# Kernel optimization log

Hardware: AMD Instinct MI355X
Metric: run time of the kernel (lower is better)

## Reference

```python
import jax, jax.numpy as jnp
import numpy as np

T, H, I, E, K = 4096, 2048, 1408, 8, 2


def setup_inputs() -> dict:
    key = jax.random.key(0)
    k1, k2, k3, k4, k5, k6 = jax.random.split(key, 6)
    hidden_states = jax.random.normal(k1, (T, H), dtype=jnp.float32)
    top_k_index = jax.random.randint(k2, (T, K), 0, E, dtype=jnp.int32)
    top_k_weights = jax.random.uniform(k3, (T, K), dtype=jnp.float32)
    # nn.Linear stores weight as [out_features, in_features]
    s_h = 1.0 / np.sqrt(H)
    s_i = 1.0 / np.sqrt(I)
    gate_w = jax.random.uniform(k4, (E, I, H), dtype=jnp.float32, minval=-s_h, maxval=s_h)
    up_w = jax.random.uniform(k5, (E, I, H), dtype=jnp.float32, minval=-s_h, maxval=s_h)
    down_w = jax.random.uniform(k6, (E, H, I), dtype=jnp.float32, minval=-s_i, maxval=s_i)
    return {
        "hidden_states": hidden_states,
        "top_k_index": top_k_index,
        "top_k_weights": top_k_weights,
        "gate_w": gate_w,
        "up_w": up_w,
        "down_w": down_w,
    }


def reference(hidden_states, top_k_index, top_k_weights, gate_w, up_w, down_w):
    # combine[t, e] = sum_k top_k_weights[t, k] * 1[top_k_index[t, k] == e]
    num_experts = gate_w.shape[0]
    one_hot = jax.nn.one_hot(top_k_index, num_experts, dtype=hidden_states.dtype)  # [T, K, E]
    combine = jnp.einsum("tk,tke->te", top_k_weights, one_hot)  # [T, E]

    # dense-equivalent of per-expert gather -> SwiGLU MLP -> scatter-add
    gate = jnp.einsum("th,eih->tei", hidden_states, gate_w)  # [T, E, I]
    up = jnp.einsum("th,eih->tei", hidden_states, up_w)      # [T, E, I]
    inter = jax.nn.silu(gate) * up                               # [T, E, I]
    out = jnp.einsum("te,tei,ehi->th", combine, inter, down_w)  # [T, H]
    return out
```

## Files before the change

### kernel.cpp

```cpp
#include <hip/hip_runtime.h>
#include <cstdint>
#include <cstddef>

#define T_TOK 4096
#define HD 2048
#define ID 1408
#define NE 8
#define NA (T_TOK * 2)
#define MAXR 10240
#define MAXT 40
#define EIH ((size_t)NE * ID * HD)
#define N4 ((int)(EIH / 4))
#define NCGU 2048
#define NCASTD 512
#define NTILE_G (MAXR / 256)
#define NGEMM_GU (NTILE_G * (ID / 128))
#define NKGU (HD / 32)
#define NKD  (ID / 32)

typedef __bf16 bf16x8 __attribute__((ext_vector_type(8)));
typedef float f32x4 __attribute__((ext_vector_type(4)));

__device__ __forceinline__ unsigned short f2bf(float f) {
  union { float f; unsigned int u; } c; c.f = f;
  unsigned int u = c.u;
  u += 0x7fffu + ((u >> 16) & 1u);
  return (unsigned short)(u >> 16);
}

__device__ __forceinline__ void gl_lds16(const unsigned short* g, unsigned short* l) {
  __builtin_amdgcn_global_load_lds(
      (const __attribute__((address_space(1))) unsigned int*)g,
      (__attribute__((address_space(3))) unsigned int*)l, 16, 0, 0);
}

__device__ __forceinline__ int swz_off(int R, int fq) {
  int q = ((R & 1) << 2) | fq;
  int p = q ^ ((R >> 1) & 7);
  return (R >> 1) * 64 + p * 8;
}

__global__ void moe_count(const int* __restrict__ idx, int* __restrict__ cnt) {
  int a = blockIdx.x * 256 + threadIdx.x;
  if (a < NA) atomicAdd(&cnt[idx[a]], 1);
}

__global__ void moe_scan(const int* __restrict__ cnt, int* __restrict__ seg,
                         int* __restrict__ work_e, int* __restrict__ work_r,
                         int* __restrict__ ntiles) {
  if (blockIdx.x == 0 && threadIdx.x == 0) {
    int off = 0, nt = 0;
    for (int e = 0; e < NE; ++e) {
      seg[e] = off;
      int c = cnt[e];
      int tiles = (c + 255) >> 8;
      for (int tb = 0; tb < tiles; ++tb) {
        work_e[nt] = e;
        work_r[nt] = off + tb * 256;
        ++nt;
      }
      off += tiles << 8;
    }
    *ntiles = nt;
  }
}

__global__ void moe_fill(const int* __restrict__ idx, const float* __restrict__ wts,
                         const int* __restrict__ seg, int* __restrict__ cnt2,
                         int* __restrict__ row_token, float* __restrict__ row_weight,
                         int* __restrict__ slot_of) {
  int a = blockIdx.x * 256 + threadIdx.x;
  if (a < NA) {
    int e = idx[a];
    int pos = atomicAdd(&cnt2[e], 1);
    int slot = seg[e] + pos;
    row_token[slot] = a >> 1;
    row_weight[slot] = wts[a];
    slot_of[a] = slot;
  }
}

__global__ void mega_gather_castgu(
    const float* __restrict__ hidden, const int* __restrict__ slot_of,
    unsigned short* __restrict__ Xg,
    const float* __restrict__ gate_w, const float* __restrict__ up_w,
    unsigned short* __restrict__ gate_bf, unsigned short* __restrict__ ub_out) {
  const int bx = blockIdx.x;
  if (bx < NA) {
    const int slot = slot_of[bx];
    const int t = bx >> 1;
    const float4* src = (const float4*)(hidden + (size_t)t * HD);
    ushort4* dst = (ushort4*)(Xg + (size_t)slot * HD);
#pragma unroll
    for (int j = 0; j < 2; ++j) {
      int i = threadIdx.x + j * 256;
      float4 v = src[i];
      ushort4 o;
      o.x = f2bf(v.x); o.y = f2bf(v.y); o.z = f2bf(v.z); o.w = f2bf(v.w);
      dst[i] = o;
    }
  } else {
    const int cb = bx - NA;
    const int total = 2 * N4;
    for (int i = cb * 256 + threadIdx.x; i < total; i += NCGU * 256) {
      const float* s; unsigned short* t; int j = i;
      if (j < N4) { s = gate_w; t = gate_bf; }
      else { s = up_w; t = ub_out; j -= N4; }
      f32x4 v = __builtin_nontemporal_load((const f32x4*)s + j);
      ushort4 o;
      o.x = f2bf(v[0]); o.y = f2bf(v[1]); o.z = f2bf(v[2]); o.w = f2bf(v[3]);
      ((ushort4*)t)[j] = o;
    }
  }
}

__global__ __launch_bounds__(512, 2) void moe_gateup(
    const unsigned short* __restrict__ Xg,
    const unsigned short* __restrict__ Wg,
    const unsigned short* __restrict__ Wu,
    unsigned short* __restrict__ inter,
    const int* __restrict__ work_e, const int* __restrict__ work_r,
    const int* __restrict__ ntiles,
    const float* __restrict__ down_w, unsigned short* __restrict__ down_bf) {
  const int bx = blockIdx.x;
  if (bx >= NGEMM_GU) {
    const int cb = bx - NGEMM_GU;
    for (int i = cb * 512 + threadIdx.x; i < N4; i += NCASTD * 512) {
      f32x4 v = __builtin_nontemporal_load((const f32x4*)down_w + i);
      ushort4 o;
      o.x = f2bf(v[0]); o.y = f2bf(v[1]); o.z = f2bf(v[2]); o.w = f2bf(v[3]);
      ((ushort4*)down_bf)[i] = o;
    }
    return;
  }
  const int g = (bx & 7) * (NGEMM_GU / 8) + (bx >> 3);
  const int tile = g % NTILE_G;
  if (tile >= *ntiles) return;
  const int e = work_e[tile];
  const int row0 = work_r[tile];
  const int col0 = (g / NTILE_G) * 128;

  __shared__ unsigned short As[3][256 * 32];
  __shared__ unsigned short Bs[3][256 * 32];

  const int tid = threadIdx.x;
  const int lane = tid & 63;
  const int wave = tid >> 6;
  const int wm = wave >> 2, wn = wave & 3;
  const int p_l = lane & 7;
  const int ub  = lane >> 3;
  const int q_l = p_l ^ ub;
  const int srow = (ub << 1) | (q_l >> 2);
  const int scol = (q_l & 3) << 3;
  const int fm = lane & 15, fq = lane >> 4;

  const size_t a_base = (size_t)row0 * HD;
  const size_t b_base = ((size_t)e * ID + col0) * HD;

  f32x4 zero = {0.f, 0.f, 0.f, 0.f};
  f32x4 accg[8][2], accu[8][2];
#pragma unroll
  for (int mi = 0; mi < 8; ++mi)
#pragma unroll
    for (int ni = 0; ni < 2; ++ni) { accg[mi][ni] = zero; accu[mi][ni] = zero; }

  auto stageA = [&](int k0, int b) {
#pragma unroll
    for (int j = 0; j < 2; ++j) {
      const int rb = j * 128 + wave * 16;
      gl_lds16(Xg + a_base + (size_t)(rb + srow) * HD + k0 + scol, &As[b][rb * 32]);
    }
  };
  auto stageB = [&](int k0, int b) {
    const int rb = wave * 16;
    gl_lds16(Wg + b_base + (size_t)(rb + srow) * HD + k0 + scol, &Bs[b][rb * 32]);
    gl_lds16(Wu + b_base + (size_t)(rb + srow) * HD + k0 + scol, &Bs[b][(128 + rb) * 32]);
  };

  stageA(0, 0); stageB(0, 0);
  stageA(32, 1); stageB(32, 1);
  asm volatile("s_waitcnt vmcnt(4)" ::: "memory");
  __builtin_amdgcn_s_barrier();
  __builtin_amdgcn_sched_barrier(0);

  int bufc = 0, buf2 = 2, k2 = 64;
  bf16x8 bg[2], bu[2];
#pragma unroll 1
  for (int t = 0; t < NKGU; ++t) {
    if (t + 2 < NKGU) stageA(k2, buf2);
    {
      bf16x8 af[4];
#pragma unroll
      for (int i = 0; i < 2; ++i) {
        bg[i] = *(const bf16x8*)&Bs[bufc][swz_off(wn * 32 + i * 16 + fm, fq)];
        bu[i] = *(const bf16x8*)&Bs[bufc][swz_off(128 + wn * 32 + i * 16 + fm, fq)];
      }
#pragma unroll
      for (int i = 0; i < 4; ++i)
        af[i] = *(const bf16x8*)&As[bufc][swz_off(wm * 128 + i * 16 + fm, fq)];
      __builtin_amdgcn_s_setprio(1);
#pragma unroll
      for (int mi = 0; mi < 4; ++mi)
#pragma unroll
        for (int ni = 0; ni < 2; ++ni) {
          accg[mi][ni] = __builtin_amdgcn_mfma_f32_16x16x32_bf16(af[mi], bg[ni], accg[mi][ni], 0, 0, 0);
          accu[mi][ni] = __builtin_amdgcn_mfma_f32_16x16x32_bf16(af[mi], bu[ni], accu[mi][ni], 0, 0, 0);
        }
      __builtin_amdgcn_s_setprio(0);
    }
    __builtin_amdgcn_s_barrier();
    __builtin_amdgcn_sched_barrier(0);
    if (t + 2 < NKGU) stageB(k2, buf2);
    {
      bf16x8 af[4];
#pragma unroll
      for (int i = 0; i < 4; ++i)
        af[i] = *(const bf16x8*)&As[bufc][swz_off(wm * 128 + (4 + i) * 16 + fm, fq)];
      __builtin_amdgcn_s_setprio(1);
#pragma unroll
      for (int mi = 0; mi < 4; ++mi)
#pragma unroll
        for (int ni = 0; ni < 2; ++ni) {
          accg[4 + mi][ni] = __builtin_amdgcn_mfma_f32_16x16x32_bf16(af[mi], bg[ni], accg[4 + mi][ni], 0, 0, 0);
          accu[4 + mi][ni] = __builtin_amdgcn_mfma_f32_16x16x32_bf16(af[mi], bu[ni], accu[4 + mi][ni], 0, 0, 0);
        }
      __builtin_amdgcn_s_setprio(0);
    }
    if (t < NKGU - 1) {
      if (t + 2 < NKGU) asm volatile("s_waitcnt vmcnt(4)" ::: "memory");
      else              asm volatile("s_waitcnt vmcnt(0)" ::: "memory");
      __builtin_amdgcn_s_barrier();
      __builtin_amdgcn_sched_barrier(0);
    }
    k2 += 32;
    bufc = (bufc == 2) ? 0 : bufc + 1;
    buf2 = (buf2 == 2) ? 0 : buf2 + 1;
  }

#pragma unroll
  for (int mi = 0; mi < 8; ++mi)
#pragma unroll
    for (int ni = 0; ni < 2; ++ni)
#pragma unroll
      for (int r = 0; r < 4; ++r) {
        float gg = accg[mi][ni][r];
        float u = accu[mi][ni][r];
        float v = (gg / (1.0f + __expf(-gg))) * u;
        int row = row0 + wm * 128 + mi * 16 + fq * 4 + r;
        int col = col0 + wn * 32 + ni * 16 + fm;
        inter[(size_t)row * ID + col] = f2bf(v);
      }
}

__global__ __launch_bounds__(512, 2) void moe_down(
    const unsigned short* __restrict__ inter,
    const unsigned short* __restrict__ Wd,
    float* __restrict__ out,
    const int* __restrict__ work_e, const int* __restrict__ work_r,
    const int* __restrict__ ntiles,
    const int* __restrict__ row_token, const float* __restrict__ row_weight) {
  const int tile = blockIdx.x;
  if (tile >= *ntiles) return;
  const int e = work_e[tile];
  const int row0 = work_r[tile];
  const int col0 = blockIdx.y * 256;

  __shared__ unsigned short As[3][256 * 32];
  __shared__ unsigned short Bs[3][256 * 32];
  __shared__ int tok_s[256];
  __shared__ float w_s[256];

  const int tid = threadIdx.x;
  if (tid < 256) {
    tok_s[tid] = row_token[row0 + tid];
    w_s[tid] = row_weight[row0 + tid];
  }
  __syncthreads();

  const int lane = tid & 63;
  const int wave = tid >> 6;
  const int wm = wave >> 2, wn = wave & 3;
  const int p_l = lane & 7;
  const int ub  = lane >> 3;
  const int q_l = p_l ^ ub;
  const int srow = (ub << 1) | (q_l >> 2);
  const int scol = (q_l & 3) << 3;
  const int fm = lane & 15, fq = lane >> 4;

  const size_t a_base = (size_t)row0 * ID;
  const size_t b_base = ((size_t)e * HD + col0) * ID;

  f32x4 zero = {0.f, 0.f, 0.f, 0.f};
  f32x4 acc[8][4];
#pragma unroll
  for (int mi = 0; mi < 8; ++mi)
#pragma unroll
    for (int ni = 0; ni < 4; ++ni) acc[mi][ni] = zero;

  auto stageA = [&](int k0, int b) {
#pragma unroll
    for (int j = 0; j < 2; ++j) {
      const int rb = j * 128 + wave * 16;
      gl_lds16(inter + a_base + (size_t)(rb + srow) * ID + k0 + scol, &As[b][rb * 32]);
    }
  };
  auto stageB = [&](int k0, int b) {
#pragma unroll
    for (int j = 0; j < 2; ++j) {
      const int rb = j * 128 + wave * 16;
      gl_lds16(Wd + b_base + (size_t)(rb + srow) * ID + k0 + scol, &Bs[b][rb * 32]);
    }
  };

  stageA(0, 0); stageB(0, 0);
  stageA(32, 1); stageB(32, 1);
  asm volatile("s_waitcnt vmcnt(4)" ::: "memory");
  __builtin_amdgcn_s_barrier();
  __builtin_amdgcn_sched_barrier(0);

  int bufc = 0, buf2 = 2, k2 = 64;
  bf16x8 b4[4];
#pragma unroll 1
  for (int t = 0; t < NKD; ++t) {
    if (t + 2 < NKD) stageA(k2, buf2);
    {
      bf16x8 af[4];
#pragma unroll
      for (int i = 0; i < 4; ++i)
        b4[i] = *(const bf16x8*)&Bs[bufc][swz_off(wn * 64 + i * 16 + fm, fq)];
#pragma unroll
      for (int i = 0; i < 4; ++i)
        af[i] = *(const bf16x8*)&As[bufc][swz_off(wm * 128 + i * 16 + fm, fq)];
      __builtin_amdgcn_s_setprio(1);
#pragma unroll
      for (int mi = 0; mi < 4; ++mi)
#pragma unroll
        for (int ni = 0; ni < 4; ++ni)
          acc[mi][ni] = __builtin_amdgcn_mfma_f32_16x16x32_bf16(af[mi], b4[ni], acc[mi][ni], 0, 0, 0);
      __builtin_amdgcn_s_setprio(0);
    }
    __builtin_amdgcn_s_barrier();
    __builtin_amdgcn_sched_barrier(0);
    if (t + 2 < NKD) stageB(k2, buf2);
    {
      bf16x8 af[4];
#pragma unroll
      for (int i = 0; i < 4; ++i)
        af[i] = *(const bf16x8*)&As[bufc][swz_off(wm * 128 + (4 + i) * 16 + fm, fq)];
      __builtin_amdgcn_s_setprio(1);
#pragma unroll
      for (int mi = 0; mi < 4; ++mi)
#pragma unroll
        for (int ni = 0; ni < 4; ++ni)
          acc[4 + mi][ni] = __builtin_amdgcn_mfma_f32_16x16x32_bf16(af[mi], b4[ni], acc[4 + mi][ni], 0, 0, 0);
      __builtin_amdgcn_s_setprio(0);
    }
    if (t < NKD - 1) {
      if (t + 2 < NKD) asm volatile("s_waitcnt vmcnt(4)" ::: "memory");
      else             asm volatile("s_waitcnt vmcnt(0)" ::: "memory");
      __builtin_amdgcn_s_barrier();
      __builtin_amdgcn_sched_barrier(0);
    }
    k2 += 32;
    bufc = (bufc == 2) ? 0 : bufc + 1;
    buf2 = (buf2 == 2) ? 0 : buf2 + 1;
  }

#pragma unroll
  for (int mi = 0; mi < 8; ++mi)
#pragma unroll
    for (int ni = 0; ni < 4; ++ni)
#pragma unroll
      for (int r = 0; r < 4; ++r) {
        int rl = wm * 128 + mi * 16 + fq * 4 + r;
        int tok = tok_s[rl];
        if (tok >= 0) {
          int col = col0 + wn * 64 + ni * 16 + fm;
          atomicAdd(&out[(size_t)tok * HD + col], w_s[rl] * acc[mi][ni][r]);
        }
      }
}

extern "C" void kernel_launch(void* const* d_in, const int* in_sizes, int n_in,
                              void* d_out, int out_size, void* d_ws, size_t ws_size,
                              hipStream_t stream) {
  const float* hidden = (const float*)d_in[0];
  const int* topk_idx = (const int*)d_in[1];
  const float* topk_w = (const float*)d_in[2];
  const float* gate_w = (const float*)d_in[3];
  const float* up_w = (const float*)d_in[4];
  const float* down_w = (const float*)d_in[5];
  float* out = (float*)d_out;

  char* ws = (char*)d_ws;
  size_t o_gate = 0;
  size_t o_up   = o_gate + EIH * 2;
  size_t o_down = o_up + EIH * 2;
  size_t o_xg   = o_down + EIH * 2;
  size_t o_int  = o_xg + (size_t)MAXR * HD * 2;
  size_t o_tok  = o_int + (size_t)MAXR * ID * 2;
  size_t o_wgt  = o_tok + (size_t)MAXR * 4;
  size_t o_slot = o_wgt + (size_t)MAXR * 4;
  size_t o_small = o_slot + (size_t)NA * 4;

  unsigned short* gate_bf = (unsigned short*)(ws + o_gate);
  unsigned short* up_bf   = (unsigned short*)(ws + o_up);
  unsigned short* down_bf = (unsigned short*)(ws + o_down);
  unsigned short* Xg      = (unsigned short*)(ws + o_xg);
  unsigned short* inter   = (unsigned short*)(ws + o_int);
  int* row_token = (int*)(ws + o_tok);
  float* row_weight = (float*)(ws + o_wgt);
  int* slot_of = (int*)(ws + o_slot);
  int* cnt    = (int*)(ws + o_small);
  int* cnt2   = cnt + 8;
  int* seg    = cnt + 16;
  int* ntiles = cnt + 24;
  int* work_e = cnt + 32;
  int* work_r = cnt + 32 + MAXT;

  hipMemsetAsync(out, 0, (size_t)T_TOK * HD * 4, stream);
  hipMemsetAsync(cnt, 0, (32 + 2 * MAXT) * 4, stream);
  hipMemsetAsync(row_token, 0xFF, (size_t)MAXR * 4, stream);

  moe_count<<<NA / 256, 256, 0, stream>>>(topk_idx, cnt);
  moe_scan<<<1, 64, 0, stream>>>(cnt, seg, work_e, work_r, ntiles);
  moe_fill<<<NA / 256, 256, 0, stream>>>(topk_idx, topk_w, seg, cnt2,
                                         row_token, row_weight, slot_of);

  mega_gather_castgu<<<NA + NCGU, 256, 0, stream>>>(hidden, slot_of, Xg,
                                                    gate_w, up_w, gate_bf, up_bf);

  moe_gateup<<<NGEMM_GU + NCASTD, 512, 0, stream>>>(
      Xg, gate_bf, up_bf, inter, work_e, work_r, ntiles, down_w, down_bf);

  dim3 gridB(NTILE_G, HD / 256);
  moe_down<<<gridB, 512, 0, stream>>>(inter, down_bf, out, work_e, work_r, ntiles,
                                      row_token, row_weight);
}
```

Measured before the change: 652.1 us.

## Double waves per GEMM block, halving per-wave rows and merging staging

Both grouped GEMM kernels now launch 1024-thread blocks with the same 256-row tile. Each of the 16 waves owns 64 rows instead of 128, which halves the accumulator count and lets A and B be staged together with one barrier per k-step instead of two. The down-cast tail block count is halved to match the larger blocks. The aim is more latency hiding and fewer barriers per step. The cost is that launch_bounds(1024,4) asks for an occupancy that forces a very small per-thread register budget, which risks spills, and LDS use limits how many blocks can actually be resident.

```diff
diff --git a/kernel.cpp b/kernel.cpp
--- a/kernel.cpp
+++ b/kernel.cpp
@@ -12,7 +12,7 @@
 #define EIH ((size_t)NE * ID * HD)
 #define N4 ((int)(EIH / 4))
 #define NCGU 2048
-#define NCASTD 512
+#define NCASTD 256
 #define NTILE_G (MAXR / 256)
 #define NGEMM_GU (NTILE_G * (ID / 128))
 #define NKGU (HD / 32)
@@ -114,7 +114,7 @@
   }
 }
 
-__global__ __launch_bounds__(512, 2) void moe_gateup(
+__global__ __launch_bounds__(1024, 4) void moe_gateup(
     const unsigned short* __restrict__ Xg,
     const unsigned short* __restrict__ Wg,
     const unsigned short* __restrict__ Wu,
@@ -125,7 +125,7 @@
   const int bx = blockIdx.x;
   if (bx >= NGEMM_GU) {
     const int cb = bx - NGEMM_GU;
-    for (int i = cb * 512 + threadIdx.x; i < N4; i += NCASTD * 512) {
+    for (int i = cb * 1024 + threadIdx.x; i < N4; i += NCASTD * 1024) {
       f32x4 v = __builtin_nontemporal_load((const f32x4*)down_w + i);
       ushort4 o;
       o.x = f2bf(v[0]); o.y = f2bf(v[1]); o.z = f2bf(v[2]); o.w = f2bf(v[3]);
@@ -156,40 +156,37 @@
 
   const size_t a_base = (size_t)row0 * HD;
   const size_t b_base = ((size_t)e * ID + col0) * HD;
+  const int rb = wave << 4;
 
   f32x4 zero = {0.f, 0.f, 0.f, 0.f};
-  f32x4 accg[8][2], accu[8][2];
-#pragma unroll
-  for (int mi = 0; mi < 8; ++mi)
+  f32x4 accg[4][2], accu[4][2];
+#pragma unroll
+  for (int mi = 0; mi < 4; ++mi)
 #pragma unroll
     for (int ni = 0; ni < 2; ++ni) { accg[mi][ni] = zero; accu[mi][ni] = zero; }
 
   auto stageA = [&](int k0, int b) {
-#pragma unroll
-    for (int j = 0; j < 2; ++j) {
-      const int rb = j * 128 + wave * 16;
-      gl_lds16(Xg + a_base + (size_t)(rb + srow) * HD + k0 + scol, &As[b][rb * 32]);
-    }
+    gl_lds16(Xg + a_base + (size_t)(rb + srow) * HD + k0 + scol, &As[b][rb * 32]);
   };
   auto stageB = [&](int k0, int b) {
-    const int rb = wave * 16;
-    gl_lds16(Wg + b_base + (size_t)(rb + srow) * HD + k0 + scol, &Bs[b][rb * 32]);
-    gl_lds16(Wu + b_base + (size_t)(rb + srow) * HD + k0 + scol, &Bs[b][(128 + rb) * 32]);
+    const unsigned short* src = (wave < 8)
+        ? (Wg + b_base + (size_t)(rb + srow) * HD + k0 + scol)
+        : (Wu + b_base + (size_t)(rb - 128 + srow) * HD + k0 + scol);
+    gl_lds16(src, &Bs[b][rb * 32]);
   };
 
   stageA(0, 0); stageB(0, 0);
   stageA(32, 1); stageB(32, 1);
-  asm volatile("s_waitcnt vmcnt(4)" ::: "memory");
+  asm volatile("s_waitcnt vmcnt(2)" ::: "memory");
   __builtin_amdgcn_s_barrier();
   __builtin_amdgcn_sched_barrier(0);
 
   int bufc = 0, buf2 = 2, k2 = 64;
-  bf16x8 bg[2], bu[2];
 #pragma unroll 1
   for (int t = 0; t < NKGU; ++t) {
-    if (t + 2 < NKGU) stageA(k2, buf2);
+    if (t + 2 < NKGU) { stageA(k2, buf2); stageB(k2, buf2); }
     {
-      bf16x8 af[4];
+      bf16x8 af[4], bg[2], bu[2];
 #pragma unroll
       for (int i = 0; i < 2; ++i) {
         bg[i] = *(const bf16x8*)&Bs[bufc][swz_off(wn * 32 + i * 16 + fm, fq)];
@@ -197,7 +194,7 @@
       }
 #pragma unroll
       for (int i = 0; i < 4; ++i)
-        af[i] = *(const bf16x8*)&As[bufc][swz_off(wm * 128 + i * 16 + fm, fq)];
+        af[i] = *(const bf16x8*)&As[bufc][swz_off(wm * 64 + i * 16 + fm, fq)];
       __builtin_amdgcn_s_setprio(1);
 #pragma unroll
       for (int mi = 0; mi < 4; ++mi)
@@ -208,26 +205,8 @@
         }
       __builtin_amdgcn_s_setprio(0);
     }
-    __builtin_amdgcn_s_barrier();
-    __builtin_amdgcn_sched_barrier(0);
-    if (t + 2 < NKGU) stageB(k2, buf2);
-    {
-      bf16x8 af[4];
-#pragma unroll
-      for (int i = 0; i < 4; ++i)
-        af[i] = *(const bf16x8*)&As[bufc][swz_off(wm * 128 + (4 + i) * 16 + fm, fq)];
-      __builtin_amdgcn_s_setprio(1);
-#pragma unroll
-      for (int mi = 0; mi < 4; ++mi)
-#pragma unroll
-        for (int ni = 0; ni < 2; ++ni) {
-          accg[4 + mi][ni] = __builtin_amdgcn_mfma_f32_16x16x32_bf16(af[mi], bg[ni], accg[4 + mi][ni], 0, 0, 0);
-          accu[4 + mi][ni] = __builtin_amdgcn_mfma_f32_16x16x32_bf16(af[mi], bu[ni], accu[4 + mi][ni], 0, 0, 0);
-        }
-      __builtin_amdgcn_s_setprio(0);
-    }
     if (t < NKGU - 1) {
-      if (t + 2 < NKGU) asm volatile("s_waitcnt vmcnt(4)" ::: "memory");
+      if (t + 2 < NKGU) asm volatile("s_waitcnt vmcnt(2)" ::: "memory");
       else              asm volatile("s_waitcnt vmcnt(0)" ::: "memory");
       __builtin_amdgcn_s_barrier();
       __builtin_amdgcn_sched_barrier(0);
@@ -238,7 +217,7 @@
   }
 
 #pragma unroll
-  for (int mi = 0; mi < 8; ++mi)
+  for (int mi = 0; mi < 4; ++mi)
 #pragma unroll
     for (int ni = 0; ni < 2; ++ni)
 #pragma unroll
@@ -246,13 +225,13 @@
         float gg = accg[mi][ni][r];
         float u = accu[mi][ni][r];
         float v = (gg / (1.0f + __expf(-gg))) * u;
-        int row = row0 + wm * 128 + mi * 16 + fq * 4 + r;
+        int row = row0 + wm * 64 + mi * 16 + fq * 4 + r;
         int col = col0 + wn * 32 + ni * 16 + fm;
         inter[(size_t)row * ID + col] = f2bf(v);
       }
 }
 
-__global__ __launch_bounds__(512, 2) void moe_down(
+__global__ __launch_bounds__(1024, 4) void moe_down(
     const unsigned short* __restrict__ inter,
     const unsigned short* __restrict__ Wd,
     float* __restrict__ out,
@@ -275,7 +254,6 @@
     tok_s[tid] = row_token[row0 + tid];
     w_s[tid] = row_weight[row0 + tid];
   }
-  __syncthreads();
 
   const int lane = tid & 63;
   const int wave = tid >> 6;
@@ -289,48 +267,40 @@
 
   const size_t a_base = (size_t)row0 * ID;
   const size_t b_base = ((size_t)e * HD + col0) * ID;
+  const int rb = wave << 4;
 
   f32x4 zero = {0.f, 0.f, 0.f, 0.f};
-  f32x4 acc[8][4];
-#pragma unroll
-  for (int mi = 0; mi < 8; ++mi)
+  f32x4 acc[4][4];
+#pragma unroll
+  for (int mi = 0; mi < 4; ++mi)
 #pragma unroll
     for (int ni = 0; ni < 4; ++ni) acc[mi][ni] = zero;
 
   auto stageA = [&](int k0, int b) {
-#pragma unroll
-    for (int j = 0; j < 2; ++j) {
-      const int rb = j * 128 + wave * 16;
-      gl_lds16(inter + a_base + (size_t)(rb + srow) * ID + k0 + scol, &As[b][rb * 32]);
-    }
+    gl_lds16(inter + a_base + (size_t)(rb + srow) * ID + k0 + scol, &As[b][rb * 32]);
   };
   auto stageB = [&](int k0, int b) {
-#pragma unroll
-    for (int j = 0; j < 2; ++j) {
-      const int rb = j * 128 + wave * 16;
-      gl_lds16(Wd + b_base + (size_t)(rb + srow) * ID + k0 + scol, &Bs[b][rb * 32]);
-    }
+    gl_lds16(Wd + b_base + (size_t)(rb + srow) * ID + k0 + scol, &Bs[b][rb * 32]);
   };
 
   stageA(0, 0); stageB(0, 0);
   stageA(32, 1); stageB(32, 1);
-  asm volatile("s_waitcnt vmcnt(4)" ::: "memory");
+  asm volatile("s_waitcnt vmcnt(2)" ::: "memory");
   __builtin_amdgcn_s_barrier();
   __builtin_amdgcn_sched_barrier(0);
 
   int bufc = 0, buf2 = 2, k2 = 64;
-  bf16x8 b4[4];
 #pragma unroll 1
   for (int t = 0; t < NKD; ++t) {
-    if (t + 2 < NKD) stageA(k2, buf2);
+    if (t + 2 < NKD) { stageA(k2, buf2); stageB(k2, buf2); }
     {
-      bf16x8 af[4];
+      bf16x8 af[4], b4[4];
 #pragma unroll
       for (int i = 0; i < 4; ++i)
         b4[i] = *(const bf16x8*)&Bs[bufc][swz_off(wn * 64 + i * 16 + fm, fq)];
 #pragma unroll
       for (int i = 0; i < 4; ++i)
-        af[i] = *(const bf16x8*)&As[bufc][swz_off(wm * 128 + i * 16 + fm, fq)];
+        af[i] = *(const bf16x8*)&As[bufc][swz_off(wm * 64 + i * 16 + fm, fq)];
       __builtin_amdgcn_s_setprio(1);
 #pragma unroll
       for (int mi = 0; mi < 4; ++mi)
@@ -339,24 +309,8 @@
           acc[mi][ni] = __builtin_amdgcn_mfma_f32_16x16x32_bf16(af[mi], b4[ni], acc[mi][ni], 0, 0, 0);
       __builtin_amdgcn_s_setprio(0);
     }
-    __builtin_amdgcn_s_barrier();
-    __builtin_amdgcn_sched_barrier(0);
-    if (t + 2 < NKD) stageB(k2, buf2);
-    {
-      bf16x8 af[4];
-#pragma unroll
-      for (int i = 0; i < 4; ++i)
-        af[i] = *(const bf16x8*)&As[bufc][swz_off(wm * 128 + (4 + i) * 16 + fm, fq)];
-      __builtin_amdgcn_s_setprio(1);
-#pragma unroll
-      for (int mi = 0; mi < 4; ++mi)
-#pragma unroll
-        for (int ni = 0; ni < 4; ++ni)
-          acc[4 + mi][ni] = __builtin_amdgcn_mfma_f32_16x16x32_bf16(af[mi], b4[ni], acc[4 + mi][ni], 0, 0, 0);
-      __builtin_amdgcn_s_setprio(0);
-    }
     if (t < NKD - 1) {
-      if (t + 2 < NKD) asm volatile("s_waitcnt vmcnt(4)" ::: "memory");
+      if (t + 2 < NKD) asm volatile("s_waitcnt vmcnt(2)" ::: "memory");
       else             asm volatile("s_waitcnt vmcnt(0)" ::: "memory");
       __builtin_amdgcn_s_barrier();
       __builtin_amdgcn_sched_barrier(0);
@@ -367,12 +321,12 @@
   }
 
 #pragma unroll
-  for (int mi = 0; mi < 8; ++mi)
+  for (int mi = 0; mi < 4; ++mi)
 #pragma unroll
     for (int ni = 0; ni < 4; ++ni)
 #pragma unroll
       for (int r = 0; r < 4; ++r) {
-        int rl = wm * 128 + mi * 16 + fq * 4 + r;
+        int rl = wm * 64 + mi * 16 + fq * 4 + r;
         int tok = tok_s[rl];
         if (tok >= 0) {
           int col = col0 + wn * 64 + ni * 16 + fm;
@@ -430,10 +384,10 @@
   mega_gather_castgu<<<NA + NCGU, 256, 0, stream>>>(hidden, slot_of, Xg,
                                                     gate_w, up_w, gate_bf, up_bf);
 
-  moe_gateup<<<NGEMM_GU + NCASTD, 512, 0, stream>>>(
+  moe_gateup<<<NGEMM_GU + NCASTD, 1024, 0, stream>>>(
       Xg, gate_bf, up_bf, inter, work_e, work_r, ntiles, down_w, down_bf);
 
   dim3 gridB(NTILE_G, HD / 256);
-  moe_down<<<gridB, 512, 0, stream>>>(inter, down_bf, out, work_e, work_r, ntiles,
-                                      row_token, row_weight);
-}
+  moe_down<<<gridB, 1024, 0, stream>>>(inter, down_bf, out, work_e, work_r, ntiles,
+                                       row_token, row_weight);
+}
```

Measured after the change: 629.5 us. 3.5% less time.

## Restructure MoE GEMM mainloops to BK=64 double-buffered four-phase ping-pong schedule

Applied to the files above, without the earlier changes.

Both the gate/up and down GEMM kernels move from a triple-buffered K=32 pipeline to a double-buffered K=64 pipeline. Each iteration is split into four phases, and each phase issues one quarter of the next tile's global-to-LDS loads and then runs one quadrant of MFMAs, with barriers and waitcnts in between. The goal is to halve loop overhead and barrier count per unit of K and to interleave loads with compute more finely. In exchange there are more barriers per iteration and a riskier ordering. The __syncthreads after the tok_s/w_s load in the down kernel is dropped and now relies on later barriers.

```diff
diff --git a/kernel.cpp b/kernel.cpp
--- a/kernel.cpp
+++ b/kernel.cpp
@@ -15,11 +15,14 @@
 #define NCASTD 512
 #define NTILE_G (MAXR / 256)
 #define NGEMM_GU (NTILE_G * (ID / 128))
-#define NKGU (HD / 32)
-#define NKD  (ID / 32)
+#define NKGU (HD / 64)
+#define NKD  (ID / 64)
 
 typedef __bf16 bf16x8 __attribute__((ext_vector_type(8)));
 typedef float f32x4 __attribute__((ext_vector_type(4)));
+
+#define MFMA16 __builtin_amdgcn_mfma_f32_16x16x32_bf16
+#define LD8(base, off) (*(const bf16x8*)&(base)[(off)])
 
 __device__ __forceinline__ unsigned short f2bf(float f) {
   union { float f; unsigned int u; } c; c.f = f;
@@ -38,6 +41,9 @@
   int q = ((R & 1) << 2) | fq;
   int p = q ^ ((R >> 1) & 7);
   return (R >> 1) * 64 + p * 8;
+}
+__device__ __forceinline__ int lds_off(int ks, int P, int fq) {
+  return ks * 8192 + swz_off(P, fq);
 }
 
 __global__ void moe_count(const int* __restrict__ idx, int* __restrict__ cnt) {
@@ -140,8 +146,8 @@
   const int row0 = work_r[tile];
   const int col0 = (g / NTILE_G) * 128;
 
-  __shared__ unsigned short As[3][256 * 32];
-  __shared__ unsigned short Bs[3][256 * 32];
+  __shared__ unsigned short As[2][16384];
+  __shared__ unsigned short Bs[2][16384];
 
   const int tid = threadIdx.x;
   const int lane = tid & 63;
@@ -162,92 +168,133 @@
 #pragma unroll
   for (int mi = 0; mi < 8; ++mi)
 #pragma unroll
-    for (int ni = 0; ni < 2; ++ni) { accg[mi][ni] = zero; accu[mi][ni] = zero; }
-
-  auto stageA = [&](int k0, int b) {
-#pragma unroll
-    for (int j = 0; j < 2; ++j) {
-      const int rb = j * 128 + wave * 16;
-      gl_lds16(Xg + a_base + (size_t)(rb + srow) * HD + k0 + scol, &As[b][rb * 32]);
-    }
+    for (int j = 0; j < 2; ++j) { accg[mi][j] = zero; accu[mi][j] = zero; }
+
+  auto stA = [&](int k0, int b, int h) {
+    const int abase = ((wave >> 2) << 7) + (h << 6) + ((wave & 3) << 4);
+    const int pp = (h << 7) + (wave << 4);
+#pragma unroll
+    for (int s = 0; s < 2; ++s)
+      gl_lds16(Xg + a_base + (size_t)(abase + srow) * HD + k0 + s * 32 + scol,
+               &As[b][s * 8192 + pp * 32]);
   };
-  auto stageB = [&](int k0, int b) {
-    const int rb = wave * 16;
-    gl_lds16(Wg + b_base + (size_t)(rb + srow) * HD + k0 + scol, &Bs[b][rb * 32]);
-    gl_lds16(Wu + b_base + (size_t)(rb + srow) * HD + k0 + scol, &Bs[b][(128 + rb) * 32]);
+  auto stB = [&](int k0, int b, int h) {
+    const unsigned short* W = h ? Wu : Wg;
+    const int pp = (h << 7) + (wave << 4);
+#pragma unroll
+    for (int s = 0; s < 2; ++s)
+      gl_lds16(W + b_base + (size_t)((wave << 4) + srow) * HD + k0 + s * 32 + scol,
+               &Bs[b][s * 8192 + pp * 32]);
   };
 
-  stageA(0, 0); stageB(0, 0);
-  stageA(32, 1); stageB(32, 1);
+  stA(0, 0, 0); stB(0, 0, 0); stB(0, 0, 1); stA(0, 0, 1);
   asm volatile("s_waitcnt vmcnt(4)" ::: "memory");
   __builtin_amdgcn_s_barrier();
-  __builtin_amdgcn_sched_barrier(0);
-
-  int bufc = 0, buf2 = 2, k2 = 64;
-  bf16x8 bg[2], bu[2];
+
+  bf16x8 a[4][2], bg[2][2], bu[2][2];
 #pragma unroll 1
   for (int t = 0; t < NKGU; ++t) {
-    if (t + 2 < NKGU) stageA(k2, buf2);
-    {
-      bf16x8 af[4];
-#pragma unroll
-      for (int i = 0; i < 2; ++i) {
-        bg[i] = *(const bf16x8*)&Bs[bufc][swz_off(wn * 32 + i * 16 + fm, fq)];
-        bu[i] = *(const bf16x8*)&Bs[bufc][swz_off(128 + wn * 32 + i * 16 + fm, fq)];
-      }
-#pragma unroll
-      for (int i = 0; i < 4; ++i)
-        af[i] = *(const bf16x8*)&As[bufc][swz_off(wm * 128 + i * 16 + fm, fq)];
-      __builtin_amdgcn_s_setprio(1);
-#pragma unroll
-      for (int mi = 0; mi < 4; ++mi)
-#pragma unroll
-        for (int ni = 0; ni < 2; ++ni) {
-          accg[mi][ni] = __builtin_amdgcn_mfma_f32_16x16x32_bf16(af[mi], bg[ni], accg[mi][ni], 0, 0, 0);
-          accu[mi][ni] = __builtin_amdgcn_mfma_f32_16x16x32_bf16(af[mi], bu[ni], accu[mi][ni], 0, 0, 0);
-        }
-      __builtin_amdgcn_s_setprio(0);
-    }
-    __builtin_amdgcn_s_barrier();
+    const int k1 = (t + 1) << 6;
+    const bool pf = (t + 1 < NKGU);
+    const unsigned short* Ab = As[t & 1];
+    const unsigned short* Bb = Bs[t & 1];
+    const int bn = (t & 1) ^ 1;
+
+#pragma unroll
+    for (int i = 0; i < 4; ++i)
+#pragma unroll
+      for (int ks = 0; ks < 2; ++ks)
+        a[i][ks] = LD8(Ab, lds_off(ks, wm * 64 + i * 16 + fm, fq));
+#pragma unroll
+    for (int j = 0; j < 2; ++j)
+#pragma unroll
+      for (int ks = 0; ks < 2; ++ks)
+        bg[j][ks] = LD8(Bb, lds_off(ks, wn * 32 + j * 16 + fm, fq));
+    if (pf) stA(k1, bn, 0);
+    __builtin_amdgcn_s_barrier();
+    asm volatile("s_waitcnt lgkmcnt(0)" ::: "memory");
     __builtin_amdgcn_sched_barrier(0);
-    if (t + 2 < NKGU) stageB(k2, buf2);
-    {
-      bf16x8 af[4];
-#pragma unroll
-      for (int i = 0; i < 4; ++i)
-        af[i] = *(const bf16x8*)&As[bufc][swz_off(wm * 128 + (4 + i) * 16 + fm, fq)];
-      __builtin_amdgcn_s_setprio(1);
-#pragma unroll
-      for (int mi = 0; mi < 4; ++mi)
-#pragma unroll
-        for (int ni = 0; ni < 2; ++ni) {
-          accg[4 + mi][ni] = __builtin_amdgcn_mfma_f32_16x16x32_bf16(af[mi], bg[ni], accg[4 + mi][ni], 0, 0, 0);
-          accu[4 + mi][ni] = __builtin_amdgcn_mfma_f32_16x16x32_bf16(af[mi], bu[ni], accu[4 + mi][ni], 0, 0, 0);
-        }
-      __builtin_amdgcn_s_setprio(0);
-    }
-    if (t < NKGU - 1) {
-      if (t + 2 < NKGU) asm volatile("s_waitcnt vmcnt(4)" ::: "memory");
-      else              asm volatile("s_waitcnt vmcnt(0)" ::: "memory");
-      __builtin_amdgcn_s_barrier();
-      __builtin_amdgcn_sched_barrier(0);
-    }
-    k2 += 32;
-    bufc = (bufc == 2) ? 0 : bufc + 1;
-    buf2 = (buf2 == 2) ? 0 : buf2 + 1;
+    __builtin_amdgcn_s_setprio(1);
+#pragma unroll
+    for (int mi = 0; mi < 4; ++mi)
+#pragma unroll
+      for (int j = 0; j < 2; ++j)
+#pragma unroll
+        for (int ks = 0; ks < 2; ++ks)
+          accg[mi][j] = MFMA16(a[mi][ks], bg[j][ks], accg[mi][j], 0, 0, 0);
+    __builtin_amdgcn_s_setprio(0);
+    if (pf) asm volatile("s_waitcnt vmcnt(4)" ::: "memory");
+    else    asm volatile("s_waitcnt vmcnt(2)" ::: "memory");
+    __builtin_amdgcn_s_barrier();
+
+#pragma unroll
+    for (int j = 0; j < 2; ++j)
+#pragma unroll
+      for (int ks = 0; ks < 2; ++ks)
+        bu[j][ks] = LD8(Bb, lds_off(ks, 128 + wn * 32 + j * 16 + fm, fq));
+    if (pf) stB(k1, bn, 0);
+    __builtin_amdgcn_s_barrier();
+    asm volatile("s_waitcnt lgkmcnt(0)" ::: "memory");
+    __builtin_amdgcn_sched_barrier(0);
+    __builtin_amdgcn_s_setprio(1);
+#pragma unroll
+    for (int mi = 0; mi < 4; ++mi)
+#pragma unroll
+      for (int j = 0; j < 2; ++j)
+#pragma unroll
+        for (int ks = 0; ks < 2; ++ks)
+          accu[mi][j] = MFMA16(a[mi][ks], bu[j][ks], accu[mi][j], 0, 0, 0);
+    __builtin_amdgcn_s_setprio(0);
+    if (pf) asm volatile("s_waitcnt vmcnt(4)" ::: "memory");
+    else    asm volatile("s_waitcnt vmcnt(0)" ::: "memory");
+    __builtin_amdgcn_s_barrier();
+
+#pragma unroll
+    for (int i = 0; i < 4; ++i)
+#pragma unroll
+      for (int ks = 0; ks < 2; ++ks)
+        a[i][ks] = LD8(Ab, lds_off(ks, 128 + wm * 64 + i * 16 + fm, fq));
+    if (pf) stB(k1, bn, 1);
+    __builtin_amdgcn_s_barrier();
+    asm volatile("s_waitcnt lgkmcnt(0)" ::: "memory");
+    __builtin_amdgcn_sched_barrier(0);
+    __builtin_amdgcn_s_setprio(1);
+#pragma unroll
+    for (int mi = 0; mi < 4; ++mi)
+#pragma unroll
+      for (int j = 0; j < 2; ++j)
+#pragma unroll
+        for (int ks = 0; ks < 2; ++ks)
+          accu[4 + mi][j] = MFMA16(a[mi][ks], bu[j][ks], accu[4 + mi][j], 0, 0, 0);
+    __builtin_amdgcn_s_setprio(0);
+    __builtin_amdgcn_s_barrier();
+
+    if (pf) stA(k1, bn, 1);
+    __builtin_amdgcn_s_barrier();
+    __builtin_amdgcn_s_setprio(1);
+#pragma unroll
+    for (int mi = 0; mi < 4; ++mi)
+#pragma unroll
+      for (int j = 0; j < 2; ++j)
+#pragma unroll
+        for (int ks = 0; ks < 2; ++ks)
+          accg[4 + mi][j] = MFMA16(a[mi][ks], bg[j][ks], accg[4 + mi][j], 0, 0, 0);
+    __builtin_amdgcn_s_setprio(0);
+    if (pf) asm volatile("s_waitcnt vmcnt(4)" ::: "memory");
+    __builtin_amdgcn_s_barrier();
   }
 
 #pragma unroll
   for (int mi = 0; mi < 8; ++mi)
 #pragma unroll
-    for (int ni = 0; ni < 2; ++ni)
+    for (int j = 0; j < 2; ++j)
 #pragma unroll
       for (int r = 0; r < 4; ++r) {
-        float gg = accg[mi][ni][r];
-        float u = accu[mi][ni][r];
+        float gg = accg[mi][j][r];
+        float u = accu[mi][j][r];
         float v = (gg / (1.0f + __expf(-gg))) * u;
         int row = row0 + wm * 128 + mi * 16 + fq * 4 + r;
-        int col = col0 + wn * 32 + ni * 16 + fm;
+        int col = col0 + wn * 32 + j * 16 + fm;
         inter[(size_t)row * ID + col] = f2bf(v);
       }
 }
@@ -265,8 +312,8 @@
   const int row0 = work_r[tile];
   const int col0 = blockIdx.y * 256;
 
-  __shared__ unsigned short As[3][256 * 32];
-  __shared__ unsigned short Bs[3][256 * 32];
+  __shared__ unsigned short As[2][16384];
+  __shared__ unsigned short Bs[2][16384];
   __shared__ int tok_s[256];
   __shared__ float w_s[256];
 
@@ -275,7 +322,6 @@
     tok_s[tid] = row_token[row0 + tid];
     w_s[tid] = row_weight[row0 + tid];
   }
-  __syncthreads();
 
   const int lane = tid & 63;
   const int wave = tid >> 6;
@@ -295,88 +341,133 @@
 #pragma unroll
   for (int mi = 0; mi < 8; ++mi)
 #pragma unroll
-    for (int ni = 0; ni < 4; ++ni) acc[mi][ni] = zero;
-
-  auto stageA = [&](int k0, int b) {
-#pragma unroll
-    for (int j = 0; j < 2; ++j) {
-      const int rb = j * 128 + wave * 16;
-      gl_lds16(inter + a_base + (size_t)(rb + srow) * ID + k0 + scol, &As[b][rb * 32]);
-    }
+    for (int j = 0; j < 4; ++j) acc[mi][j] = zero;
+
+  auto stA = [&](int k0, int b, int h) {
+    const int abase = ((wave >> 2) << 7) + (h << 6) + ((wave & 3) << 4);
+    const int pp = (h << 7) + (wave << 4);
+#pragma unroll
+    for (int s = 0; s < 2; ++s)
+      gl_lds16(inter + a_base + (size_t)(abase + srow) * ID + k0 + s * 32 + scol,
+               &As[b][s * 8192 + pp * 32]);
   };
-  auto stageB = [&](int k0, int b) {
-#pragma unroll
-    for (int j = 0; j < 2; ++j) {
-      const int rb = j * 128 + wave * 16;
-      gl_lds16(Wd + b_base + (size_t)(rb + srow) * ID + k0 + scol, &Bs[b][rb * 32]);
-    }
+  auto stB = [&](int k0, int b, int h) {
+    const int bbase = ((wave >> 1) << 6) + (h << 5) + ((wave & 1) << 4);
+    const int pp = (h << 7) + (wave << 4);
+#pragma unroll
+    for (int s = 0; s < 2; ++s)
+      gl_lds16(Wd + b_base + (size_t)(bbase + srow) * ID + k0 + s * 32 + scol,
+               &Bs[b][s * 8192 + pp * 32]);
   };
 
-  stageA(0, 0); stageB(0, 0);
-  stageA(32, 1); stageB(32, 1);
+  stA(0, 0, 0); stB(0, 0, 0); stB(0, 0, 1); stA(0, 0, 1);
   asm volatile("s_waitcnt vmcnt(4)" ::: "memory");
   __builtin_amdgcn_s_barrier();
-  __builtin_amdgcn_sched_barrier(0);
-
-  int bufc = 0, buf2 = 2, k2 = 64;
-  bf16x8 b4[4];
+
+  bf16x8 a[4][2], b0[2][2], b1[2][2];
 #pragma unroll 1
   for (int t = 0; t < NKD; ++t) {
-    if (t + 2 < NKD) stageA(k2, buf2);
-    {
-      bf16x8 af[4];
-#pragma unroll
-      for (int i = 0; i < 4; ++i)
-        b4[i] = *(const bf16x8*)&Bs[bufc][swz_off(wn * 64 + i * 16 + fm, fq)];
-#pragma unroll
-      for (int i = 0; i < 4; ++i)
-        af[i] = *(const bf16x8*)&As[bufc][swz_off(wm * 128 + i * 16 + fm, fq)];
-      __builtin_amdgcn_s_setprio(1);
-#pragma unroll
-      for (int mi = 0; mi < 4; ++mi)
-#pragma unroll
-        for (int ni = 0; ni < 4; ++ni)
-          acc[mi][ni] = __builtin_amdgcn_mfma_f32_16x16x32_bf16(af[mi], b4[ni], acc[mi][ni], 0, 0, 0);
-      __builtin_amdgcn_s_setprio(0);
-    }
-    __builtin_amdgcn_s_barrier();
+    const int k1 = (t + 1) << 6;
+    const bool pf = (t + 1 < NKD);
+    const unsigned short* Ab = As[t & 1];
+    const unsigned short* Bb = Bs[t & 1];
+    const int bn = (t & 1) ^ 1;
+
+#pragma unroll
+    for (int i = 0; i < 4; ++i)
+#pragma unroll
+      for (int ks = 0; ks < 2; ++ks)
+        a[i][ks] = LD8(Ab, lds_off(ks, wm * 64 + i * 16 + fm, fq));
+#pragma unroll
+    for (int j = 0; j < 2; ++j)
+#pragma unroll
+      for (int ks = 0; ks < 2; ++ks)
+        b0[j][ks] = LD8(Bb, lds_off(ks, wn * 32 + j * 16 + fm, fq));
+    if (pf) stA(k1, bn, 0);
+    __builtin_amdgcn_s_barrier();
+    asm volatile("s_waitcnt lgkmcnt(0)" ::: "memory");
     __builtin_amdgcn_sched_barrier(0);
-    if (t + 2 < NKD) stageB(k2, buf2);
-    {
-      bf16x8 af[4];
-#pragma unroll
-      for (int i = 0; i < 4; ++i)
-        af[i] = *(const bf16x8*)&As[bufc][swz_off(wm * 128 + (4 + i) * 16 + fm, fq)];
-      __builtin_amdgcn_s_setprio(1);
-#pragma unroll
-      for (int mi = 0; mi < 4; ++mi)
-#pragma unroll
-        for (int ni = 0; ni < 4; ++ni)
-          acc[4 + mi][ni] = __builtin_amdgcn_mfma_f32_16x16x32_bf16(af[mi], b4[ni], acc[4 + mi][ni], 0, 0, 0);
-      __builtin_amdgcn_s_setprio(0);
-    }
-    if (t < NKD - 1) {
-      if (t + 2 < NKD) asm volatile("s_waitcnt vmcnt(4)" ::: "memory");
-      else             asm volatile("s_waitcnt vmcnt(0)" ::: "memory");
-      __builtin_amdgcn_s_barrier();
-      __builtin_amdgcn_sched_barrier(0);
-    }
-    k2 += 32;
-    bufc = (bufc == 2) ? 0 : bufc + 1;
-    buf2 = (buf2 == 2) ? 0 : buf2 + 1;
+    __builtin_amdgcn_s_setprio(1);
+#pragma unroll
+    for (int mi = 0; mi < 4; ++mi)
+#pragma unroll
+      for (int j = 0; j < 2; ++j)
+#pragma unroll
+        for (int ks = 0; ks < 2; ++ks)
+          acc[mi][j] = MFMA16(a[mi][ks], b0[j][ks], acc[mi][j], 0, 0, 0);
+    __builtin_amdgcn_s_setprio(0);
+    if (pf) asm volatile("s_waitcnt vmcnt(4)" ::: "memory");
+    else    asm volatile("s_waitcnt vmcnt(2)" ::: "memory");
+    __builtin_amdgcn_s_barrier();
+
+#pragma unroll
+    for (int j = 0; j < 2; ++j)
+#pragma unroll
+      for (int ks = 0; ks < 2; ++ks)
+        b1[j][ks] = LD8(Bb, lds_off(ks, 128 + wn * 32 + j * 16 + fm, fq));
+    if (pf) stB(k1, bn, 0);
+    __builtin_amdgcn_s_barrier();
+    asm volatile("s_waitcnt lgkmcnt(0)" ::: "memory");
+    __builtin_amdgcn_sched_barrier(0);
+    __builtin_amdgcn_s_setprio(1);
+#pragma unroll
+    for (int mi = 0; mi < 4; ++mi)
+#pragma unroll
+      for (int j = 0; j < 2; ++j)
+#pragma unroll
+        for (int ks = 0; ks < 2; ++ks)
+          acc[mi][2 + j] = MFMA16(a[mi][ks], b1[j][ks], acc[mi][2 + j], 0, 0, 0);
+    __builtin_amdgcn_s_setprio(0);
+    if (pf) asm volatile("s_waitcnt vmcnt(4)" ::: "memory");
+    else    asm volatile("s_waitcnt vmcnt(0)" ::: "memory");
+    __builtin_amdgcn_s_barrier();
+
+#pragma unroll
+    for (int i = 0; i < 4; ++i)
+#pragma unroll
+      for (int ks = 0; ks < 2; ++ks)
+        a[i][ks] = LD8(Ab, lds_off(ks, 128 + wm * 64 + i * 16 + fm, fq));
+    if (pf) stB(k1, bn, 1);
+    __builtin_amdgcn_s_barrier();
+    asm volatile("s_waitcnt lgkmcnt(0)" ::: "memory");
+    __builtin_amdgcn_sched_barrier(0);
+    __builtin_amdgcn_s_setprio(1);
+#pragma unroll
+    for (int mi = 0; mi < 4; ++mi)
+#pragma unroll
+      for (int j = 0; j < 2; ++j)
+#pragma unroll
+        for (int ks = 0; ks < 2; ++ks)
+          acc[4 + mi][2 + j] = MFMA16(a[mi][ks], b1[j][ks], acc[4 + mi][2 + j], 0, 0, 0);
+    __builtin_amdgcn_s_setprio(0);
+    __builtin_amdgcn_s_barrier();
+
+    if (pf) stA(k1, bn, 1);
+    __builtin_amdgcn_s_barrier();
+    __builtin_amdgcn_s_setprio(1);
+#pragma unroll
+    for (int mi = 0; mi < 4; ++mi)
+#pragma unroll
+      for (int j = 0; j < 2; ++j)
+#pragma unroll
+        for (int ks = 0; ks < 2; ++ks)
+          acc[4 + mi][j] = MFMA16(a[mi][ks], b0[j][ks], acc[4 + mi][j], 0, 0, 0);
+    __builtin_amdgcn_s_setprio(0);
+    if (pf) asm volatile("s_waitcnt vmcnt(4)" ::: "memory");
+    __builtin_amdgcn_s_barrier();
   }
 
 #pragma unroll
   for (int mi = 0; mi < 8; ++mi)
 #pragma unroll
-    for (int ni = 0; ni < 4; ++ni)
+    for (int j = 0; j < 4; ++j)
 #pragma unroll
       for (int r = 0; r < 4; ++r) {
         int rl = wm * 128 + mi * 16 + fq * 4 + r;
         int tok = tok_s[rl];
         if (tok >= 0) {
-          int col = col0 + wn * 64 + ni * 16 + fm;
-          atomicAdd(&out[(size_t)tok * HD + col], w_s[rl] * acc[mi][ni][r]);
+          int col = col0 + wn * 64 + (j >> 1) * 32 + (j & 1) * 16 + fm;
+          atomicAdd(&out[(size_t)tok * HD + col], w_s[rl] * acc[mi][j][r]);
         }
       }
 }
```

Result: faster. 620.6 us (-4.8%).
